# Performance work log

Measured on AMD Instinct MI355X. Metric: run time of the kernel, lower is better.

Reference implementation:

```python
import jax, jax.numpy as jnp
import numpy as np

B, S, E, H = 32, 256, 768, 32
D = E // H  # head_dim = 24


def setup_inputs() -> dict:
    key = jax.random.key(0)
    ks = jax.random.split(key, 10)
    w_sc = 1.0 / np.sqrt(E)  # xavier-ish init scale for weights
    return {
        "feats": jax.random.normal(ks[0], (B, S, E), jnp.float32),
        "attn_bias": jax.random.normal(ks[1], (B, H, S, S), jnp.float32),
        "delta_pos": jax.random.normal(ks[2], (B, S, S, 3), jnp.float32),
        "Wq": jax.random.normal(ks[3], (E, E), jnp.float32) * w_sc,
        "bq": jnp.zeros((E,), jnp.float32),
        "Wk": jax.random.normal(ks[4], (E, E), jnp.float32) * w_sc,
        "bk": jnp.zeros((E,), jnp.float32),
        "Wv": jax.random.normal(ks[5], (E, E), jnp.float32) * w_sc,
        "bv": jnp.zeros((E,), jnp.float32),
        "Wfx": jax.random.normal(ks[6], (E,), jnp.float32) * w_sc,
        "Wfy": jax.random.normal(ks[7], (E,), jnp.float32) * w_sc,
        "Wfz": jax.random.normal(ks[8], (E,), jnp.float32) * w_sc,
    }


def reference(feats, attn_bias, delta_pos, Wq, bq, Wk, bk, Wv, bv, Wfx, Wfy, Wfz):
    b, s, e = feats.shape
    h = attn_bias.shape[1]
    d = e // h
    scaling = d ** -0.5
    # q/k/v projections; q scaled by 1/sqrt(head_dim)
    q = ((feats @ Wq + bq) * scaling).reshape(b, s, h, d).transpose(0, 2, 1, 3)  # (b,h,s,d)
    k = (feats @ Wk + bk).reshape(b, s, h, d).transpose(0, 2, 1, 3)              # (b,h,t,d)
    v = (feats @ Wv + bv).reshape(b, s, h, d).transpose(0, 2, 1, 3)              # (b,h,t,d)
    scores = jnp.einsum('bhsd,bhtd->bhst', q, k) + attn_bias
    probs = jax.nn.softmax(scores, axis=-1)  # dropout p in eval -> identity
    # rot_attn_probs = probs[...,None] * delta_pos[:,None] fused into one contraction:
    # (b,h,s,t) * (b,s,t,3) contracted with (b,h,t,c) over t -> (b,s,3,h,c)
    attn = jnp.einsum('bhst,bstx,bhtc->bsxhc', probs, delta_pos, v)
    attn = attn.reshape(b, s, 3, e)  # flatten (h,c) -> e
    out_x = attn[..., 0, :] @ Wfx  # (b,s)
    out_y = attn[..., 1, :] @ Wfy
    out_z = attn[..., 2, :] @ Wfz
    return jnp.stack([out_x, out_y, out_z], axis=-1)  # (b,s,3)
```

## Files before the change

kernel.cpp:

```cpp
#include <hip/hip_runtime.h>
#include <hip/hip_bf16.h>

#define B_ 32
#define S_ 256
#define E_ 768
#define H_ 32
#define D_ 24
#define NTOT 1664
#define LK 40

typedef __hip_bfloat16 bf16;
typedef __attribute__((ext_vector_type(8))) short short8;
typedef __attribute__((ext_vector_type(4))) float floatx4;
typedef __attribute__((ext_vector_type(2))) float f32x2;

__global__ __launch_bounds__(256) void cast_feats(
    const float* __restrict__ in, bf16* __restrict__ outp, int n4)
{
  int i = blockIdx.x * 256 + threadIdx.x;
  if (i < n4) {
    float4 v = reinterpret_cast<const float4*>(in)[i];
    union { ushort4 u; bf16 b[4]; } pk;
    pk.b[0] = (bf16)v.x; pk.b[1] = (bf16)v.y;
    pk.b[2] = (bf16)v.z; pk.b[3] = (bf16)v.w;
    reinterpret_cast<ushort4*>(outp)[i] = pk.u;
  }
}

__global__ __launch_bounds__(256) void prep_pack(
    const float* __restrict__ Wq, const float* __restrict__ Wk,
    const float* __restrict__ Wv,
    const float* __restrict__ bq, const float* __restrict__ bk,
    const float* __restrict__ bv,
    const float* __restrict__ Wfx, const float* __restrict__ Wfy,
    const float* __restrict__ Wfz,
    bf16* __restrict__ Wt, float* __restrict__ biasf)
{
  const float qscale = 0.20412414523193154f;
  int gid = blockIdx.x * 256 + threadIdx.x;
  if (gid < NTOT * E_) {
    int n = gid / E_, k = gid % E_;
    float val;
    if (n < 768) {
      val = Wq[(size_t)k * E_ + n] * qscale;
    } else if (n < 1536) {
      val = Wk[(size_t)k * E_ + (n - 768)];
    } else if (n < 1632) {
      int nn = n - 1536, x = nn >> 5, h = nn & 31;
      const float* Wf = (x == 0) ? Wfx : (x == 1 ? Wfy : Wfz);
      float s = 0.f;
      #pragma unroll
      for (int c = 0; c < D_; c++)
        s += Wv[(size_t)k * E_ + h * D_ + c] * Wf[h * D_ + c];
      val = s;
    } else {
      val = 0.f;
    }
    Wt[gid] = (bf16)val;
  } else {
    int n = gid - NTOT * E_;
    if (n < NTOT) {
      float val;
      if (n < 768) {
        val = bq[n] * qscale;
      } else if (n < 1536) {
        val = bk[n - 768];
      } else if (n < 1632) {
        int nn = n - 1536, x = nn >> 5, h = nn & 31;
        const float* Wf = (x == 0) ? Wfx : (x == 1 ? Wfy : Wfz);
        float s = 0.f;
        #pragma unroll
        for (int c = 0; c < D_; c++)
          s += bv[h * D_ + c] * Wf[h * D_ + c];
        val = s;
      } else {
        val = 0.f;
      }
      biasf[n] = val;
    }
  }
}

__global__ __launch_bounds__(256) void gemm_qkv(
    const bf16* __restrict__ A, const bf16* __restrict__ Wt,
    const float* __restrict__ biasf,
    bf16* __restrict__ qout, bf16* __restrict__ kout,
    float* __restrict__ vwout)
{
  __shared__ __align__(16) short As[128 * LK];
  __shared__ __align__(16) short Bs[128 * LK];
  int tid = threadIdx.x;
  int m0 = blockIdx.y * 128, n0 = blockIdx.x * 128;
  int lrow = tid >> 2, lcol = (tid & 3) * 8;
  int wave = tid >> 6, lane = tid & 63;
  int wm = (wave >> 1) * 64, wn = (wave & 1) * 64;
  int fr = lane & 15, quad = lane >> 4;

  floatx4 acc[4][4];
  const floatx4 zero = {0.f, 0.f, 0.f, 0.f};
  #pragma unroll
  for (int i = 0; i < 4; i++)
    #pragma unroll
    for (int j = 0; j < 4; j++) acc[i][j] = zero;

  const bf16* Aptr = A + (size_t)(m0 + lrow) * E_ + lcol;
  const bf16* Bptr = Wt + (size_t)(n0 + lrow) * E_ + lcol;
  float4 av0 = *reinterpret_cast<const float4*>(Aptr);
  float4 av1 = *reinterpret_cast<const float4*>(Aptr + (size_t)64 * E_);
  float4 bv0 = *reinterpret_cast<const float4*>(Bptr);
  float4 bv1 = *reinterpret_cast<const float4*>(Bptr + (size_t)64 * E_);

  for (int k0 = 0; k0 < E_; k0 += 32) {
    __syncthreads();
    *reinterpret_cast<float4*>(&As[lrow * LK + lcol]) = av0;
    *reinterpret_cast<float4*>(&As[(lrow + 64) * LK + lcol]) = av1;
    *reinterpret_cast<float4*>(&Bs[lrow * LK + lcol]) = bv0;
    *reinterpret_cast<float4*>(&Bs[(lrow + 64) * LK + lcol]) = bv1;
    __syncthreads();
    if (k0 + 32 < E_) {
      av0 = *reinterpret_cast<const float4*>(Aptr + k0 + 32);
      av1 = *reinterpret_cast<const float4*>(Aptr + (size_t)64 * E_ + k0 + 32);
      bv0 = *reinterpret_cast<const float4*>(Bptr + k0 + 32);
      bv1 = *reinterpret_cast<const float4*>(Bptr + (size_t)64 * E_ + k0 + 32);
    }
    short8 af[4], bfr[4];
    #pragma unroll
    for (int t = 0; t < 4; t++)
      af[t] = *reinterpret_cast<const short8*>(
          &As[(wm + t * 16 + fr) * LK + quad * 8]);
    #pragma unroll
    for (int t = 0; t < 4; t++)
      bfr[t] = *reinterpret_cast<const short8*>(
          &Bs[(wn + t * 16 + fr) * LK + quad * 8]);
    #pragma unroll
    for (int ti = 0; ti < 4; ti++)
      #pragma unroll
      for (int tj = 0; tj < 4; tj++)
        acc[ti][tj] = __builtin_amdgcn_mfma_f32_16x16x32_bf16(
            af[ti], bfr[tj], acc[ti][tj], 0, 0, 0);
  }

  #pragma unroll
  for (int ti = 0; ti < 4; ti++) {
    #pragma unroll
    for (int tj = 0; tj < 4; tj++) {
      int n = n0 + wn + tj * 16 + fr;
      float bias = biasf[n];
      #pragma unroll
      for (int r = 0; r < 4; r++) {
        int m = m0 + wm + ti * 16 + quad * 4 + r;
        int b = m >> 8, s = m & 255;
        float val = acc[ti][tj][r] + bias;
        if (n < 768) {
          int h = n / 24, d = n - h * 24;
          qout[(((size_t)b * H_ + h) * S_ + s) * D_ + d] = (bf16)val;
        } else if (n < 1536) {
          int n2 = n - 768;
          int h = n2 / 24, d = n2 - h * 24;
          kout[(((size_t)b * H_ + h) * S_ + s) * D_ + d] = (bf16)val;
        } else if (n < 1632) {
          int nn = n - 1536, x = nn >> 5, h = nn & 31;
          vwout[(((size_t)x * B_ + b) * H_ + h) * S_ + s] = val;
        }
      }
    }
  }
}

__global__ __launch_bounds__(256) void attn_kernel(
    const bf16* __restrict__ qg, const bf16* __restrict__ kg,
    const float* __restrict__ vwg, const float* __restrict__ biasg,
    const float* __restrict__ dpg, float* __restrict__ out)
{
  __shared__ __align__(16) float kv[S_][28];
  int bh = blockIdx.x;
  int b = bh >> 5, h = bh & 31;
  int s = threadIdx.x;

  {
    const short8* kr8 = reinterpret_cast<const short8*>(
        kg + ((size_t)bh * S_ + s) * D_);
    #pragma unroll
    for (int i = 0; i < 3; i++) {
      short8 kk = kr8[i];
      float4 f0, f1;
      union { short u; bf16 bb; } cv;
      cv.u = kk[0]; f0.x = (float)cv.bb;
      cv.u = kk[1]; f0.y = (float)cv.bb;
      cv.u = kk[2]; f0.z = (float)cv.bb;
      cv.u = kk[3]; f0.w = (float)cv.bb;
      cv.u = kk[4]; f1.x = (float)cv.bb;
      cv.u = kk[5]; f1.y = (float)cv.bb;
      cv.u = kk[6]; f1.z = (float)cv.bb;
      cv.u = kk[7]; f1.w = (float)cv.bb;
      *reinterpret_cast<float4*>(&kv[s][i * 8]) = f0;
      *reinterpret_cast<float4*>(&kv[s][i * 8 + 4]) = f1;
    }
    float4 vwp;
    vwp.x = vwg[(((size_t)0 * B_ + b) * H_ + h) * S_ + s];
    vwp.y = vwg[(((size_t)1 * B_ + b) * H_ + h) * S_ + s];
    vwp.z = vwg[(((size_t)2 * B_ + b) * H_ + h) * S_ + s];
    vwp.w = 0.f;
    *reinterpret_cast<float4*>(&kv[s][24]) = vwp;
  }

  f32x2 qd[12];
  {
    const short8* qr8 = reinterpret_cast<const short8*>(
        qg + ((size_t)bh * S_ + s) * D_);
    #pragma unroll
    for (int i = 0; i < 3; i++) {
      short8 qq = qr8[i];
      #pragma unroll
      for (int j = 0; j < 4; j++) {
        union { short u; bf16 bb; } a, c;
        a.u = qq[2 * j]; c.u = qq[2 * j + 1];
        f32x2 t2; t2.x = (float)a.bb; t2.y = (float)c.bb;
        qd[i * 4 + j] = t2;
      }
    }
  }
  __syncthreads();

  const float* biasp = biasg + (size_t)bh * S_ * S_ + (size_t)s * S_;
  const float* dpp   = dpg + (size_t)(b * S_ + s) * S_ * 3;

  float l = 0.f, ax = 0.f, ay = 0.f, az = 0.f;

  auto group = [&](int tb, float4 bias4, float4 d0, float4 d1, float4 d2) {
    float dx[4] = {d0.x, d0.w, d1.z, d2.y};
    float dy[4] = {d0.y, d1.x, d1.w, d2.z};
    float dz[4] = {d0.z, d1.y, d2.x, d2.w};
    float bb[4] = {bias4.x, bias4.y, bias4.z, bias4.w};
    #pragma unroll
    for (int j = 0; j < 4; j++) {
      const float4* krow4 = reinterpret_cast<const float4*>(&kv[tb + j][0]);
      f32x2 acc2; acc2.x = 0.f; acc2.y = 0.f;
      #pragma unroll
      for (int i = 0; i < 6; i++) {
        float4 k4 = krow4[i];
        f32x2 klo; klo.x = k4.x; klo.y = k4.y;
        f32x2 khi; khi.x = k4.z; khi.y = k4.w;
        acc2 += qd[2 * i] * klo;
        acc2 += qd[2 * i + 1] * khi;
      }
      float4 vw4 = krow4[6];
      float sc = acc2.x + acc2.y + (bb[j] - 4.0f);
      float p = __expf(sc);
      l += p;
      ax = fmaf(p * dx[j], vw4.x, ax);
      ay = fmaf(p * dy[j], vw4.y, ay);
      az = fmaf(p * dz[j], vw4.z, az);
    }
  };

  float4 nb0 = *reinterpret_cast<const float4*>(biasp);
  float4 nb1 = *reinterpret_cast<const float4*>(biasp + 4);
  float4 ne0 = *reinterpret_cast<const float4*>(dpp);
  float4 ne1 = *reinterpret_cast<const float4*>(dpp + 4);
  float4 ne2 = *reinterpret_cast<const float4*>(dpp + 8);
  float4 ne3 = *reinterpret_cast<const float4*>(dpp + 12);
  float4 ne4 = *reinterpret_cast<const float4*>(dpp + 16);
  float4 ne5 = *reinterpret_cast<const float4*>(dpp + 20);

  for (int t0 = 0; t0 < S_; t0 += 8) {
    float4 b0 = nb0, b1 = nb1;
    float4 e0 = ne0, e1 = ne1, e2 = ne2, e3 = ne3, e4 = ne4, e5 = ne5;
    int tn = (t0 + 8 < S_) ? t0 + 8 : 0;
    nb0 = *reinterpret_cast<const float4*>(biasp + tn);
    nb1 = *reinterpret_cast<const float4*>(biasp + tn + 4);
    const float* dpn = dpp + (size_t)tn * 3;
    ne0 = *reinterpret_cast<const float4*>(dpn);
    ne1 = *reinterpret_cast<const float4*>(dpn + 4);
    ne2 = *reinterpret_cast<const float4*>(dpn + 8);
    ne3 = *reinterpret_cast<const float4*>(dpn + 12);
    ne4 = *reinterpret_cast<const float4*>(dpn + 16);
    ne5 = *reinterpret_cast<const float4*>(dpn + 20);

    group(t0, b0, e0, e1, e2);
    group(t0 + 4, b1, e3, e4, e5);
  }

  float inv = 1.0f / l;
  float* op = out + (size_t)(b * S_ + s) * 3;
  atomicAdd(op + 0, ax * inv);
  atomicAdd(op + 1, ay * inv);
  atomicAdd(op + 2, az * inv);
}

extern "C" void kernel_launch(void* const* d_in, const int* in_sizes, int n_in,
                              void* d_out, int out_size, void* d_ws, size_t ws_size,
                              hipStream_t stream)
{
  const float* feats     = (const float*)d_in[0];
  const float* attn_bias = (const float*)d_in[1];
  const float* delta_pos = (const float*)d_in[2];
  const float* Wq        = (const float*)d_in[3];
  const float* bq        = (const float*)d_in[4];
  const float* Wk        = (const float*)d_in[5];
  const float* bk        = (const float*)d_in[6];
  const float* Wv        = (const float*)d_in[7];
  const float* bv        = (const float*)d_in[8];
  const float* Wfx       = (const float*)d_in[9];
  const float* Wfy       = (const float*)d_in[10];
  const float* Wfz       = (const float*)d_in[11];

  char* ws = (char*)d_ws;
  size_t off = 0;
  auto alloc = [&](size_t bytes) -> void* {
    void* p = ws + off;
    off = (off + bytes + 255) & ~(size_t)255;
    return p;
  };
  bf16*  ws_fb   = (bf16*) alloc((size_t)B_ * S_ * E_ * 2);
  bf16*  ws_q    = (bf16*) alloc((size_t)B_ * H_ * S_ * D_ * 2);
  bf16*  ws_k    = (bf16*) alloc((size_t)B_ * H_ * S_ * D_ * 2);
  float* ws_vw   = (float*)alloc((size_t)3 * B_ * H_ * S_ * 4);
  bf16*  ws_Wt   = (bf16*) alloc((size_t)NTOT * E_ * 2);
  float* ws_bias = (float*)alloc((size_t)NTOT * 4);

  hipMemsetAsync(d_out, 0, (size_t)B_ * S_ * 3 * 4, stream);

  int n4 = B_ * S_ * E_ / 4;
  cast_feats<<<(n4 + 255) / 256, 256, 0, stream>>>(feats, ws_fb, n4);

  int prep_n = NTOT * E_ + NTOT;
  prep_pack<<<(prep_n + 255) / 256, 256, 0, stream>>>(
      Wq, Wk, Wv, bq, bk, bv, Wfx, Wfy, Wfz, ws_Wt, ws_bias);

  gemm_qkv<<<dim3(NTOT / 128, B_ * S_ / 128), 256, 0, stream>>>(
      ws_fb, ws_Wt, ws_bias, ws_q, ws_k, ws_vw);

  attn_kernel<<<B_ * H_, 256, 0, stream>>>(ws_q, ws_k, ws_vw, attn_bias,
                                           delta_pos, (float*)d_out);
}
```

Measured before the change: 610.4 us.

## Reorder attention blocks by batch-minor, widen load batches, replace atomics with reduction kernel

```diff
diff --git a/kernel.cpp b/kernel.cpp
--- a/kernel.cpp
+++ b/kernel.cpp
@@ -170,11 +170,12 @@
 __global__ __launch_bounds__(256) void attn_kernel(
     const bf16* __restrict__ qg, const bf16* __restrict__ kg,
     const float* __restrict__ vwg, const float* __restrict__ biasg,
-    const float* __restrict__ dpg, float* __restrict__ out)
+    const float* __restrict__ dpg, float* __restrict__ part)
 {
   __shared__ __align__(16) float kv[S_][28];
-  int bh = blockIdx.x;
-  int b = bh >> 5, h = bh & 31;
+  int blk = blockIdx.x;
+  int b = blk & 31, h = blk >> 5;
+  int bh = b * H_ + h;
   int s = threadIdx.x;
 
   {
@@ -227,14 +228,20 @@
 
   float l = 0.f, ax = 0.f, ay = 0.f, az = 0.f;
 
-  auto group = [&](int tb, float4 bias4, float4 d0, float4 d1, float4 d2) {
-    float dx[4] = {d0.x, d0.w, d1.z, d2.y};
-    float dy[4] = {d0.y, d1.x, d1.w, d2.z};
-    float dz[4] = {d0.z, d1.y, d2.x, d2.w};
-    float bb[4] = {bias4.x, bias4.y, bias4.z, bias4.w};
-    #pragma unroll
-    for (int j = 0; j < 4; j++) {
-      const float4* krow4 = reinterpret_cast<const float4*>(&kv[tb + j][0]);
+  for (int t0 = 0; t0 < S_; t0 += 16) {
+    union { float4 v4[4]; float f[16]; } bb;
+    #pragma unroll
+    for (int i = 0; i < 4; i++)
+      bb.v4[i] = *reinterpret_cast<const float4*>(biasp + t0 + 4 * i);
+    union { float4 v4[12]; float f[48]; } dd;
+    const float* dpc = dpp + (size_t)t0 * 3;
+    #pragma unroll
+    for (int i = 0; i < 12; i++)
+      dd.v4[i] = *reinterpret_cast<const float4*>(dpc + 4 * i);
+
+    #pragma unroll
+    for (int j = 0; j < 16; j++) {
+      const float4* krow4 = reinterpret_cast<const float4*>(&kv[t0 + j][0]);
       f32x2 acc2; acc2.x = 0.f; acc2.y = 0.f;
       #pragma unroll
       for (int i = 0; i < 6; i++) {
@@ -245,47 +252,33 @@
         acc2 += qd[2 * i + 1] * khi;
       }
       float4 vw4 = krow4[6];
-      float sc = acc2.x + acc2.y + (bb[j] - 4.0f);
+      float sc = acc2.x + acc2.y + (bb.f[j] - 4.0f);
       float p = __expf(sc);
       l += p;
-      ax = fmaf(p * dx[j], vw4.x, ax);
-      ay = fmaf(p * dy[j], vw4.y, ay);
-      az = fmaf(p * dz[j], vw4.z, az);
-    }
-  };
-
-  float4 nb0 = *reinterpret_cast<const float4*>(biasp);
-  float4 nb1 = *reinterpret_cast<const float4*>(biasp + 4);
-  float4 ne0 = *reinterpret_cast<const float4*>(dpp);
-  float4 ne1 = *reinterpret_cast<const float4*>(dpp + 4);
-  float4 ne2 = *reinterpret_cast<const float4*>(dpp + 8);
-  float4 ne3 = *reinterpret_cast<const float4*>(dpp + 12);
-  float4 ne4 = *reinterpret_cast<const float4*>(dpp + 16);
-  float4 ne5 = *reinterpret_cast<const float4*>(dpp + 20);
-
-  for (int t0 = 0; t0 < S_; t0 += 8) {
-    float4 b0 = nb0, b1 = nb1;
-    float4 e0 = ne0, e1 = ne1, e2 = ne2, e3 = ne3, e4 = ne4, e5 = ne5;
-    int tn = (t0 + 8 < S_) ? t0 + 8 : 0;
-    nb0 = *reinterpret_cast<const float4*>(biasp + tn);
-    nb1 = *reinterpret_cast<const float4*>(biasp + tn + 4);
-    const float* dpn = dpp + (size_t)tn * 3;
-    ne0 = *reinterpret_cast<const float4*>(dpn);
-    ne1 = *reinterpret_cast<const float4*>(dpn + 4);
-    ne2 = *reinterpret_cast<const float4*>(dpn + 8);
-    ne3 = *reinterpret_cast<const float4*>(dpn + 12);
-    ne4 = *reinterpret_cast<const float4*>(dpn + 16);
-    ne5 = *reinterpret_cast<const float4*>(dpn + 20);
-
-    group(t0, b0, e0, e1, e2);
-    group(t0 + 4, b1, e3, e4, e5);
+      ax = fmaf(p * dd.f[3 * j + 0], vw4.x, ax);
+      ay = fmaf(p * dd.f[3 * j + 1], vw4.y, ay);
+      az = fmaf(p * dd.f[3 * j + 2], vw4.z, az);
+    }
   }
 
   float inv = 1.0f / l;
-  float* op = out + (size_t)(b * S_ + s) * 3;
-  atomicAdd(op + 0, ax * inv);
-  atomicAdd(op + 1, ay * inv);
-  atomicAdd(op + 2, az * inv);
+  float* op = part + ((size_t)bh * S_ + s) * 3;
+  op[0] = ax * inv;
+  op[1] = ay * inv;
+  op[2] = az * inv;
+}
+
+__global__ __launch_bounds__(256) void reduce_h(
+    const float* __restrict__ part, float* __restrict__ out)
+{
+  int k = blockIdx.x * 256 + threadIdx.x;
+  int b = k / (S_ * 3);
+  int r = k - b * (S_ * 3);
+  const float* p = part + (size_t)b * H_ * S_ * 3 + r;
+  float acc = 0.f;
+  #pragma unroll
+  for (int h = 0; h < H_; h++) acc += p[(size_t)h * S_ * 3];
+  out[k] = acc;
 }
 
 extern "C" void kernel_launch(void* const* d_in, const int* in_sizes, int n_in,
@@ -318,8 +311,7 @@
   float* ws_vw   = (float*)alloc((size_t)3 * B_ * H_ * S_ * 4);
   bf16*  ws_Wt   = (bf16*) alloc((size_t)NTOT * E_ * 2);
   float* ws_bias = (float*)alloc((size_t)NTOT * 4);
-
-  hipMemsetAsync(d_out, 0, (size_t)B_ * S_ * 3 * 4, stream);
+  float* ws_part = (float*)alloc((size_t)B_ * H_ * S_ * 3 * 4);
 
   int n4 = B_ * S_ * E_ / 4;
   cast_feats<<<(n4 + 255) / 256, 256, 0, stream>>>(feats, ws_fb, n4);
@@ -332,5 +324,7 @@
       ws_fb, ws_Wt, ws_bias, ws_q, ws_k, ws_vw);
 
   attn_kernel<<<B_ * H_, 256, 0, stream>>>(ws_q, ws_k, ws_vw, attn_bias,
-                                           delta_pos, (float*)d_out);
-}
+                                           delta_pos, ws_part);
+
+  reduce_h<<<(B_ * S_ * 3) / 256, 256, 0, stream>>>(ws_part, (float*)d_out);
+}
```

Result: slower. 646.9 us (+6.0%).
